# Performance work log

Hardware: AMD Instinct MI355X
Metric: run time of the kernel (lower is better)

Reference implementation:

```python
import jax, jax.numpy as jnp
import numpy as np

N_NODES = 50000


def _gcn_norm(edge_index, num_nodes):
    """PyG GCNConv normalization: add self-loops, symmetric deg^{-1/2} weights."""
    loops = jnp.arange(num_nodes, dtype=edge_index.dtype)
    src = jnp.concatenate([edge_index[0], loops])
    dst = jnp.concatenate([edge_index[1], loops])
    deg = jax.ops.segment_sum(jnp.ones_like(dst, dtype=jnp.float32), dst,
                              num_segments=num_nodes)
    dinv = jax.lax.rsqrt(jnp.maximum(deg, 1.0))  # self-loops guarantee deg>=1
    norm = dinv[src] * dinv[dst]                 # [E + N]
    return src, dst, norm


def _gcn_conv(x, W, b, src, dst, norm, num_nodes):
    h = x @ W                                    # [N, out] dense GEMM
    msg = h[src] * norm[:, None]                 # gather + scale
    agg = jax.ops.segment_sum(msg, dst, num_segments=num_nodes)
    return agg + b


def setup_inputs() -> dict:
    key = jax.random.key(0)
    ks = jax.random.split(key, 8)
    d = 128
    scale = 1.0 / np.sqrt(d)
    emb = jax.random.normal(ks[0], (N_NODES, d), dtype=jnp.float32)
    W1 = jax.random.normal(ks[1], (d, d), dtype=jnp.float32) * scale
    W2 = jax.random.normal(ks[2], (d, d), dtype=jnp.float32) * scale
    W3 = jax.random.normal(ks[3], (d, d), dtype=jnp.float32) * scale
    b1 = jnp.zeros((d,), dtype=jnp.float32)
    b2 = jnp.zeros((d,), dtype=jnp.float32)
    b3 = jnp.zeros((d,), dtype=jnp.float32)
    edge_index = jax.random.randint(ks[4], (2, 600000), 0, N_NODES, dtype=jnp.int64)
    return {"emb": emb, "W1": W1, "b1": b1, "W2": W2, "b2": b2,
            "W3": W3, "b3": b3, "edge_index": edge_index}


def reference(emb, W1, b1, W2, b2, W3, b3, edge_index):
    # Eval-mode forward: F.dropout(training=False) is identity.
    src, dst, norm = _gcn_norm(edge_index, N_NODES)
    x = emb
    x = jax.nn.relu(_gcn_conv(x, W1, b1, src, dst, norm, N_NODES))
    x = jax.nn.relu(_gcn_conv(x, W2, b2, src, dst, norm, N_NODES))
    x = _gcn_conv(x, W3, b3, src, dst, norm, N_NODES)
    x = x.at[0].set(0.0)  # x[0] = zeros(x.shape[1])
    return x
```

## Files before the change

### kernel.cpp

```cpp
#include <hip/hip_runtime.h>
#include <hip/hip_fp16.h>

#define NN 50000
#define D 128
#define SCAN_BS 512

typedef __attribute__((ext_vector_type(8))) short bf16x8;
typedef __attribute__((ext_vector_type(16))) float f32x16;
typedef _Float16 h16;
typedef __attribute__((ext_vector_type(2))) _Float16 h16x2;
typedef __attribute__((ext_vector_type(8))) _Float16 h16x8;

struct alignas(16) S8 { short s[8]; };

static __device__ __forceinline__ short bf16_rne(float f) {
    unsigned u = __float_as_uint(f);
    unsigned r = (u + 0x7FFFu + ((u >> 16) & 1u)) >> 16;
    return (short)r;
}


__global__ void count_kernel(const int* __restrict__ dst, int* __restrict__ cnt, int E) {
    int e = blockIdx.x * blockDim.x + threadIdx.x;
    if (e < E) atomicAdd(&cnt[dst[e]], 1);
}

__global__ __launch_bounds__(SCAN_BS) void scan1_kernel(const int* __restrict__ cnt,
                                                        int* __restrict__ rs,
                                                        int* __restrict__ bsum,
                                                        float* __restrict__ dinv, int n) {
    __shared__ int sm[SCAN_BS];
    int i = blockIdx.x * SCAN_BS + threadIdx.x;
    int c = (i < n - 1) ? cnt[i] : 0;
    int v = (c + 3) & ~3;
    if (i < n - 1) dinv[i] = rsqrtf((float)c + 1.0f);
    sm[threadIdx.x] = v;
    __syncthreads();
#pragma unroll
    for (int off = 1; off < SCAN_BS; off <<= 1) {
        int t = 0;
        if ((int)threadIdx.x >= off) t = sm[threadIdx.x - off];
        __syncthreads();
        if ((int)threadIdx.x >= off) sm[threadIdx.x] += t;
        __syncthreads();
    }
    int incl = sm[threadIdx.x];
    if (i < n) rs[i] = incl - v;
    if (threadIdx.x == SCAN_BS - 1) bsum[blockIdx.x] = incl;
}

__global__ __launch_bounds__(SCAN_BS) void scan3_kernel(int* __restrict__ rs,
                                                        const int* __restrict__ bsum,
                                                        int* __restrict__ cursor,
                                                        const int* __restrict__ cnt,
                                                        int2* __restrict__ csr2,
                                                        int n, int g) {
    __shared__ int sm[128];
    int t = threadIdx.x;
    if (t < 128) sm[t] = (t < g) ? bsum[t] : 0;
    __syncthreads();
#pragma unroll
    for (int off = 1; off < 128; off <<= 1) {
        int tv = 0;
        if (t >= off && t < 128) tv = sm[t - off];
        __syncthreads();
        if (t >= off && t < 128) sm[t] += tv;
        __syncthreads();
    }
    int own = ((int)blockIdx.x < g) ? bsum[blockIdx.x] : 0;
    int add = sm[blockIdx.x] - own;
    int i = blockIdx.x * SCAN_BS + t;
    if (i < n) {
        int val = rs[i] + add;
        rs[i] = val;
        if (i < n - 1) {
            cursor[i] = val;
            int c = cnt[i];
            int pc = (c + 3) & ~3;
            for (int j = val + c; j < val + pc; j++) csr2[j] = make_int2(0, 0);
        }
    }
}

__global__ void scatter_kernel(const int* __restrict__ srcA, const int* __restrict__ dstA,
                               const float* __restrict__ dinv, int* __restrict__ cursor,
                               int2* __restrict__ csr2, int E) {
    int e = blockIdx.x * blockDim.x + threadIdx.x;
    if (e < E) {
        int d = dstA[e];
        int s = srcA[e];
        int pos = atomicAdd(&cursor[d], 1);
        csr2[pos] = make_int2(s, __float_as_int(dinv[s]));
    }
}

__global__ __launch_bounds__(256, 2) void gemm_mfma(const void* __restrict__ Xv, int x_is_f32,
                                                    const float* __restrict__ W,
                                                    h16* __restrict__ H, int M,
                                                    int* __restrict__ cnt_zero) {
    __shared__ short Ws[32768];
    {
        const int l  = threadIdx.x & 63;
        const int ct = threadIdx.x >> 6;
        const int n  = ct * 32 + (l & 31);
        const int lh = l >> 5;
#pragma unroll
        for (int ks = 0; ks < 8; ks++) {
            const int kbase = ks * 16 + lh * 8;
            S8 hi8, lo8;
#pragma unroll
            for (int j = 0; j < 8; j++) {
                float w = W[(kbase + j) * D + n];
                short hi = bf16_rne(w);
                float hif = __uint_as_float(((unsigned)(unsigned short)hi) << 16);
                hi8.s[j] = hi;
                lo8.s[j] = (short)(__float_as_uint(w - hif) >> 16);
            }
            const int base = ((ks * 4 + ct) * 64 + l) * 8;
            *(S8*)(Ws + base)         = hi8;
            *(S8*)(Ws + base + 16384) = lo8;
        }
        if (cnt_zero && blockIdx.x < 196) {
            int i = blockIdx.x * 256 + threadIdx.x;
            if (i < NN + 1) cnt_zero[i] = 0;
        }
    }
    __syncthreads();

    const int wave = threadIdx.x >> 6;
    const int lane = threadIdx.x & 63;
    const int row0 = blockIdx.x * 128 + wave * 32;
    const int arow = min(row0 + (lane & 31), M - 1);
    const int koff = (lane >> 5) * 8;

    f32x16 acc[4] = {};

#pragma unroll
    for (int ks = 0; ks < 8; ks++) {
        float f[8];
        if (x_is_f32) {
            const float* p = (const float*)Xv + (size_t)arow * D + koff + ks * 16;
            float4 fa = *(const float4*)p;
            float4 fb = *(const float4*)(p + 4);
            f[0] = fa.x; f[1] = fa.y; f[2] = fa.z; f[3] = fa.w;
            f[4] = fb.x; f[5] = fb.y; f[6] = fb.z; f[7] = fb.w;
        } else {
            const h16* p = (const h16*)Xv + (size_t)arow * D + koff + ks * 16;
            h16x8 hv = *(const h16x8*)p;
#pragma unroll
            for (int j = 0; j < 8; j++) f[j] = (float)hv[j];
        }
        bf16x8 ahi, alo;
#pragma unroll
        for (int j = 0; j < 8; j++) {
            unsigned u = __float_as_uint(f[j]);
            ahi[j] = (short)(u >> 16);
            float l = f[j] - __uint_as_float(u & 0xFFFF0000u);
            alo[j] = (short)(__float_as_uint(l) >> 16);
        }
#pragma unroll
        for (int ct = 0; ct < 4; ct++) {
            const int base = ((ks * 4 + ct) * 64 + lane) * 8;
            bf16x8 bhi = *(const bf16x8*)(Ws + base);
            bf16x8 blo = *(const bf16x8*)(Ws + base + 16384);
            acc[ct] = __builtin_amdgcn_mfma_f32_32x32x16_bf16(ahi, bhi, acc[ct], 0, 0, 0);
            acc[ct] = __builtin_amdgcn_mfma_f32_32x32x16_bf16(ahi, blo, acc[ct], 0, 0, 0);
            acc[ct] = __builtin_amdgcn_mfma_f32_32x32x16_bf16(alo, bhi, acc[ct], 0, 0, 0);
        }
    }

    const int col0 = lane & 31;
    const int rbase = row0 + 4 * (lane >> 5);
#pragma unroll
    for (int ct = 0; ct < 4; ct++) {
#pragma unroll
        for (int r = 0; r < 16; r++) {
            int row = rbase + (r & 3) + 8 * (r >> 2);
            if (row < M) H[(size_t)row * D + ct * 32 + col0] = (h16)acc[ct][r];
        }
    }
}

__global__ __launch_bounds__(256) void agg_kernel(const h16* __restrict__ H,
                                                  const float* __restrict__ dinv,
                                                  const int* __restrict__ rowstart,
                                                  const int2* __restrict__ csr2,
                                                  const float* __restrict__ bias,
                                                  h16* __restrict__ out16,
                                                  float* __restrict__ out32,
                                                  int n, int mode) {
    int node = blockIdx.x * 4 + (threadIdx.x >> 6);
    if (node >= n) return;
    int lane = threadIdx.x & 63;
    int col = lane * 2;

    float di = dinv[node];
    h16x2 hs = *(const h16x2*)(H + (size_t)node * D + col);
    float ax = di * (float)hs[0];
    float ay = di * (float)hs[1];
    float bx = 0.f, by = 0.f;

    int s = __builtin_amdgcn_readfirstlane(rowstart[node]);
    int e = __builtin_amdgcn_readfirstlane(rowstart[node + 1]);

    for (int p = s; p < e; p += 4) {
        int2 w0 = csr2[p];
        int2 w1 = csr2[p + 1];
        int2 w2 = csr2[p + 2];
        int2 w3 = csr2[p + 3];
        h16x2 v0 = *(const h16x2*)(H + (size_t)w0.x * D + col);
        h16x2 v1 = *(const h16x2*)(H + (size_t)w1.x * D + col);
        h16x2 v2 = *(const h16x2*)(H + (size_t)w2.x * D + col);
        h16x2 v3 = *(const h16x2*)(H + (size_t)w3.x * D + col);
        float f0 = __int_as_float(w0.y), f1 = __int_as_float(w1.y);
        float f2 = __int_as_float(w2.y), f3 = __int_as_float(w3.y);
        ax = fmaf(f0, (float)v0[0], ax); ay = fmaf(f0, (float)v0[1], ay);
        bx = fmaf(f1, (float)v1[0], bx); by = fmaf(f1, (float)v1[1], by);
        ax = fmaf(f2, (float)v2[0], ax); ay = fmaf(f2, (float)v2[1], ay);
        bx = fmaf(f3, (float)v3[0], bx); by = fmaf(f3, (float)v3[1], by);
    }
    ax += bx; ay += by;

    float2 bb = *(const float2*)(bias + col);
    float rx = fmaf(di, ax, bb.x);
    float ry = fmaf(di, ay, bb.y);
    if (mode == 0) {
        rx = fmaxf(rx, 0.f); ry = fmaxf(ry, 0.f);
        h16x2 o; o[0] = (h16)rx; o[1] = (h16)ry;
        *(h16x2*)(out16 + (size_t)node * D + col) = o;
    } else {
        if (node == 0) { rx = 0.f; ry = 0.f; }
        *(float2*)(out32 + (size_t)node * D + col) = make_float2(rx, ry);
    }
}


extern "C" void kernel_launch(void* const* d_in, const int* in_sizes, int n_in,
                              void* d_out, int out_size, void* d_ws, size_t ws_size,
                              hipStream_t stream) {
    const float* emb = (const float*)d_in[0];
    const float* W1  = (const float*)d_in[1];
    const float* b1  = (const float*)d_in[2];
    const float* W2  = (const float*)d_in[3];
    const float* b2  = (const float*)d_in[4];
    const float* W3  = (const float*)d_in[5];
    const float* b3  = (const float*)d_in[6];
    const int*   ei  = (const int*)d_in[7];

    const int E = in_sizes[7] / 2;
    const int* srcA = ei;
    const int* dstA = ei + E;
    float* out = (float*)d_out;

    char* ws = (char*)d_ws;
    size_t off = 0;
    auto alloc = [&](size_t bytes) -> void* {
        void* p = ws + off;
        off = (off + bytes + 255) & ~(size_t)255;
        return p;
    };
    h16* h      = (h16*)alloc((size_t)NN * D * 2);
    h16* x16    = (h16*)alloc((size_t)NN * D * 2);
    float* dinv = (float*)alloc((size_t)NN * 4);
    int* cnt      = (int*)alloc((size_t)(NN + 1) * 4);
    int* rowstart = (int*)alloc((size_t)(NN + 1) * 4);
    int* cursor   = (int*)alloc((size_t)NN * 4);
    int2* csr2    = (int2*)alloc(((size_t)E + 3 * NN + 64) * 8);
    int* bsum     = (int*)alloc(256 * 4);

    const int T = 256;
    const int n_scan = NN + 1;
    const int scan_grid = (n_scan + SCAN_BS - 1) / SCAN_BS;
    const int gemm_grid = (NN + 127) / 128;
    const int agg_grid  = (NN + 3) / 4;

    gemm_mfma<<<gemm_grid, T, 0, stream>>>(emb, 1, W1, h, NN, cnt);
    count_kernel<<<(E + T - 1) / T, T, 0, stream>>>(dstA, cnt, E);
    scan1_kernel<<<scan_grid, SCAN_BS, 0, stream>>>(cnt, rowstart, bsum, dinv, n_scan);
    scan3_kernel<<<scan_grid, SCAN_BS, 0, stream>>>(rowstart, bsum, cursor, cnt, csr2,
                                                    n_scan, scan_grid);
    scatter_kernel<<<(E + T - 1) / T, T, 0, stream>>>(srcA, dstA, dinv, cursor, csr2, E);
    agg_kernel<<<agg_grid, T, 0, stream>>>(h, dinv, rowstart, csr2, b1, x16, nullptr, NN, 0);
    gemm_mfma<<<gemm_grid, T, 0, stream>>>(x16, 0, W2, h, NN, nullptr);
    agg_kernel<<<agg_grid, T, 0, stream>>>(h, dinv, rowstart, csr2, b2, x16, nullptr, NN, 0);
    gemm_mfma<<<gemm_grid, T, 0, stream>>>(x16, 0, W3, h, NN, nullptr);
    agg_kernel<<<agg_grid, T, 0, stream>>>(h, dinv, rowstart, csr2, b3, nullptr, out, NN, 1);
}
```

Measured before the change: 274.2 us.

## Switch split-precision GEMM to fp16 MFMA and fold self-loops into CSR

The GEMM now uses fp16 MFMA with hi/lo splitting instead of bf16. Because layer-2/3 inputs are already fp16, the activation low part is dropped and those layers use two MFMAs per tile instead of three, cutting MFMA work and conversion instructions. The self-loop is stored as an explicit CSR entry (padding grows by one slot per node), so the aggregation kernel no longer loads its own row separately. Risks are fp16 range limits on weights and activations, and slightly more CSR traffic.

```diff
diff --git a/kernel.cpp b/kernel.cpp
--- a/kernel.cpp
+++ b/kernel.cpp
@@ -5,19 +5,12 @@
 #define D 128
 #define SCAN_BS 512
 
-typedef __attribute__((ext_vector_type(8))) short bf16x8;
 typedef __attribute__((ext_vector_type(16))) float f32x16;
 typedef _Float16 h16;
 typedef __attribute__((ext_vector_type(2))) _Float16 h16x2;
 typedef __attribute__((ext_vector_type(8))) _Float16 h16x8;
 
-struct alignas(16) S8 { short s[8]; };
-
-static __device__ __forceinline__ short bf16_rne(float f) {
-    unsigned u = __float_as_uint(f);
-    unsigned r = (u + 0x7FFFu + ((u >> 16) & 1u)) >> 16;
-    return (short)r;
-}
+struct alignas(16) H8 { h16 h[8]; };
 
 
 __global__ void count_kernel(const int* __restrict__ dst, int* __restrict__ cnt, int E) {
@@ -32,7 +25,7 @@
     __shared__ int sm[SCAN_BS];
     int i = blockIdx.x * SCAN_BS + threadIdx.x;
     int c = (i < n - 1) ? cnt[i] : 0;
-    int v = (c + 3) & ~3;
+    int v = (i < n - 1) ? ((c + 4) & ~3) : 0;
     if (i < n - 1) dinv[i] = rsqrtf((float)c + 1.0f);
     sm[threadIdx.x] = v;
     __syncthreads();
@@ -53,6 +46,7 @@
                                                         const int* __restrict__ bsum,
                                                         int* __restrict__ cursor,
                                                         const int* __restrict__ cnt,
+                                                        const float* __restrict__ dinv,
                                                         int2* __restrict__ csr2,
                                                         int n, int g) {
     __shared__ int sm[128];
@@ -76,8 +70,9 @@
         if (i < n - 1) {
             cursor[i] = val;
             int c = cnt[i];
-            int pc = (c + 3) & ~3;
-            for (int j = val + c; j < val + pc; j++) csr2[j] = make_int2(0, 0);
+            int pc = (c + 4) & ~3;
+            csr2[val + c] = make_int2(i, __float_as_int(dinv[i]));
+            for (int j = val + c + 1; j < val + pc; j++) csr2[j] = make_int2(0, 0);
         }
     }
 }
@@ -98,7 +93,7 @@
                                                     const float* __restrict__ W,
                                                     h16* __restrict__ H, int M,
                                                     int* __restrict__ cnt_zero) {
-    __shared__ short Ws[32768];
+    __shared__ h16 Ws[32768];
     {
         const int l  = threadIdx.x & 63;
         const int ct = threadIdx.x >> 6;
@@ -107,18 +102,17 @@
 #pragma unroll
         for (int ks = 0; ks < 8; ks++) {
             const int kbase = ks * 16 + lh * 8;
-            S8 hi8, lo8;
+            H8 hi8, lo8;
 #pragma unroll
             for (int j = 0; j < 8; j++) {
                 float w = W[(kbase + j) * D + n];
-                short hi = bf16_rne(w);
-                float hif = __uint_as_float(((unsigned)(unsigned short)hi) << 16);
-                hi8.s[j] = hi;
-                lo8.s[j] = (short)(__float_as_uint(w - hif) >> 16);
+                h16 hi = (h16)w;
+                hi8.h[j] = hi;
+                lo8.h[j] = (h16)(w - (float)hi);
             }
             const int base = ((ks * 4 + ct) * 64 + l) * 8;
-            *(S8*)(Ws + base)         = hi8;
-            *(S8*)(Ws + base + 16384) = lo8;
+            *(H8*)(Ws + base)         = hi8;
+            *(H8*)(Ws + base + 16384) = lo8;
         }
         if (cnt_zero && blockIdx.x < 196) {
             int i = blockIdx.x * 256 + threadIdx.x;
@@ -137,35 +131,31 @@
 
 #pragma unroll
     for (int ks = 0; ks < 8; ks++) {
-        float f[8];
+        h16x8 ahi, alo;
         if (x_is_f32) {
             const float* p = (const float*)Xv + (size_t)arow * D + koff + ks * 16;
             float4 fa = *(const float4*)p;
             float4 fb = *(const float4*)(p + 4);
-            f[0] = fa.x; f[1] = fa.y; f[2] = fa.z; f[3] = fa.w;
-            f[4] = fb.x; f[5] = fb.y; f[6] = fb.z; f[7] = fb.w;
+            float f[8] = {fa.x, fa.y, fa.z, fa.w, fb.x, fb.y, fb.z, fb.w};
+#pragma unroll
+            for (int j = 0; j < 8; j++) {
+                h16 hi = (h16)f[j];
+                ahi[j] = hi;
+                alo[j] = (h16)(f[j] - (float)hi);
+            }
         } else {
             const h16* p = (const h16*)Xv + (size_t)arow * D + koff + ks * 16;
-            h16x8 hv = *(const h16x8*)p;
-#pragma unroll
-            for (int j = 0; j < 8; j++) f[j] = (float)hv[j];
-        }
-        bf16x8 ahi, alo;
-#pragma unroll
-        for (int j = 0; j < 8; j++) {
-            unsigned u = __float_as_uint(f[j]);
-            ahi[j] = (short)(u >> 16);
-            float l = f[j] - __uint_as_float(u & 0xFFFF0000u);
-            alo[j] = (short)(__float_as_uint(l) >> 16);
+            ahi = *(const h16x8*)p;
         }
 #pragma unroll
         for (int ct = 0; ct < 4; ct++) {
             const int base = ((ks * 4 + ct) * 64 + lane) * 8;
-            bf16x8 bhi = *(const bf16x8*)(Ws + base);
-            bf16x8 blo = *(const bf16x8*)(Ws + base + 16384);
-            acc[ct] = __builtin_amdgcn_mfma_f32_32x32x16_bf16(ahi, bhi, acc[ct], 0, 0, 0);
-            acc[ct] = __builtin_amdgcn_mfma_f32_32x32x16_bf16(ahi, blo, acc[ct], 0, 0, 0);
-            acc[ct] = __builtin_amdgcn_mfma_f32_32x32x16_bf16(alo, bhi, acc[ct], 0, 0, 0);
+            h16x8 bhi = *(const h16x8*)(Ws + base);
+            h16x8 blo = *(const h16x8*)(Ws + base + 16384);
+            acc[ct] = __builtin_amdgcn_mfma_f32_32x32x16_f16(ahi, bhi, acc[ct], 0, 0, 0);
+            acc[ct] = __builtin_amdgcn_mfma_f32_32x32x16_f16(ahi, blo, acc[ct], 0, 0, 0);
+            if (x_is_f32)
+                acc[ct] = __builtin_amdgcn_mfma_f32_32x32x16_f16(alo, bhi, acc[ct], 0, 0, 0);
         }
     }
 
@@ -194,11 +184,7 @@
     int lane = threadIdx.x & 63;
     int col = lane * 2;
 
-    float di = dinv[node];
-    h16x2 hs = *(const h16x2*)(H + (size_t)node * D + col);
-    float ax = di * (float)hs[0];
-    float ay = di * (float)hs[1];
-    float bx = 0.f, by = 0.f;
+    float ax = 0.f, ay = 0.f, bx = 0.f, by = 0.f;
 
     int s = __builtin_amdgcn_readfirstlane(rowstart[node]);
     int e = __builtin_amdgcn_readfirstlane(rowstart[node + 1]);
@@ -221,6 +207,7 @@
     }
     ax += bx; ay += by;
 
+    float di = dinv[node];
     float2 bb = *(const float2*)(bias + col);
     float rx = fmaf(di, ax, bb.x);
     float ry = fmaf(di, ay, bb.y);
@@ -265,7 +252,7 @@
     int* cnt      = (int*)alloc((size_t)(NN + 1) * 4);
     int* rowstart = (int*)alloc((size_t)(NN + 1) * 4);
     int* cursor   = (int*)alloc((size_t)NN * 4);
-    int2* csr2    = (int2*)alloc(((size_t)E + 3 * NN + 64) * 8);
+    int2* csr2    = (int2*)alloc(((size_t)E + 4 * NN + 64) * 8);
     int* bsum     = (int*)alloc(256 * 4);
 
     const int T = 256;
@@ -277,7 +264,7 @@
     gemm_mfma<<<gemm_grid, T, 0, stream>>>(emb, 1, W1, h, NN, cnt);
     count_kernel<<<(E + T - 1) / T, T, 0, stream>>>(dstA, cnt, E);
     scan1_kernel<<<scan_grid, SCAN_BS, 0, stream>>>(cnt, rowstart, bsum, dinv, n_scan);
-    scan3_kernel<<<scan_grid, SCAN_BS, 0, stream>>>(rowstart, bsum, cursor, cnt, csr2,
+    scan3_kernel<<<scan_grid, SCAN_BS, 0, stream>>>(rowstart, bsum, cursor, cnt, dinv, csr2,
                                                     n_scan, scan_grid);
     scatter_kernel<<<(E + T - 1) / T, T, 0, stream>>>(srcA, dstA, dinv, cursor, csr2, E);
     agg_kernel<<<agg_grid, T, 0, stream>>>(h, dinv, rowstart, csr2, b1, x16, nullptr, NN, 0);
```

New measurement: 276.9 us. About the same (+1.0%).
